# Kernel optimization log

Hardware: AMD Instinct MI355X
Metric: run time of the kernel (lower is better)

## Reference

```python
import jax, jax.numpy as jnp
import numpy as np

N = 100000
K = 16
C_IN = 64
C_MID = 64   # max(in_channels, out_channels // 2)
C_OUT = 128
EPS = 1e-5


def setup_inputs() -> dict:
    key = jax.random.key(0)
    ks = jax.random.split(key, 4)
    feat = jax.random.normal(ks[0], (N, C_IN), dtype=jnp.float32)
    reference_index = jax.random.randint(ks[1], (N, K), 0, N, dtype=jnp.int64)
    # Kaiming-ish init for the two Linear layers (torch Linear default scale)
    W1 = jax.random.normal(ks[2], (C_IN, C_MID), dtype=jnp.float32) / np.sqrt(C_IN)
    W2 = jax.random.normal(ks[3], (C_MID, C_OUT), dtype=jnp.float32) / np.sqrt(C_MID)
    return {
        "feat": feat,
        "reference_index": reference_index,
        "W1": W1,
        "b1": jnp.zeros((C_MID,), jnp.float32),
        "gamma1": jnp.ones((C_MID,), jnp.float32),
        "beta1": jnp.zeros((C_MID,), jnp.float32),
        "W2": W2,
        "b2": jnp.zeros((C_OUT,), jnp.float32),
        "gamma2": jnp.ones((C_OUT,), jnp.float32),
        "beta2": jnp.zeros((C_OUT,), jnp.float32),
    }


def _bn(x, gamma, beta):
    # BatchNorm1d in training mode: biased batch stats over the row dim.
    mean = jnp.mean(x, axis=0)
    var = jnp.var(x, axis=0)
    return (x - mean) * jax.lax.rsqrt(var + EPS) * gamma + beta


def reference(feat, reference_index, W1, b1, gamma1, beta1, W2, b2, gamma2, beta2):
    # grouping (with_xyz=False): gather neighbor features -> [N, K, C_IN]
    grouped = feat[reference_index]
    x = grouped.reshape(-1, C_IN)                 # [N*K, C_IN]
    h = jax.nn.relu(_bn(x @ W1 + b1, gamma1, beta1))   # [N*K, C_MID]
    h = jax.nn.relu(_bn(h @ W2 + b2, gamma2, beta2))   # [N*K, C_OUT]
    out = h.reshape(N, K, C_OUT).max(axis=1)      # max-pool over neighbors
    return out
```

## Files before the change

kernel.cpp:

```cpp
#include <hip/hip_runtime.h>
#include <hip/hip_bf16.h>

#define N_PTS 100000
#define KNN   16
#define NK    (N_PTS * KNN)
#define CIN   64
#define CMID  64
#define COUT  128

#define HSLC    64
#define SEG_CNT 25000
#define SEG_U32 12500

#define OFF_PC    0
#define OFF_HB    0
#define OFF_Z1B   25600000
#define OFF_CNT   38400000
#define OFF_STATS 38800000
#define OFF_W2BF  38801536
#define OFF_W1BF  38817920

typedef __attribute__((ext_vector_type(8))) short bf16x8;
typedef __attribute__((ext_vector_type(4))) float f32x4;
union U8 { uint4 u; bf16x8 v; unsigned short s[8]; };

__device__ __forceinline__ unsigned short f2bf(float f) {
    unsigned u = __float_as_uint(f);
    unsigned r = (u + 0x7fffu + ((u >> 16) & 1u)) >> 16;
    return (unsigned short)r;
}

__global__ __launch_bounds__(256) void hist_k(const int* __restrict__ idx,
                                              unsigned short* __restrict__ pc) {
    __shared__ unsigned int smem[SEG_U32];
    int seg  = blockIdx.x & 3;
    int slc  = blockIdx.x >> 2;
    int base = seg * SEG_CNT;

    for (int i = threadIdx.x; i < SEG_U32; i += 256) smem[i] = 0;
    __syncthreads();

    const int4* ip = (const int4*)idx;
    const int per = NK / 4 / HSLC;
    int s = slc * per, e = s + per;
    for (int i = s + threadIdx.x; i < e; i += 256) {
        int4 v = ip[i];
        int a;
        a = v.x - base; if ((unsigned)a < (unsigned)SEG_CNT)
            atomicAdd(&smem[a >> 1], 1u << ((a & 1) * 16));
        a = v.y - base; if ((unsigned)a < (unsigned)SEG_CNT)
            atomicAdd(&smem[a >> 1], 1u << ((a & 1) * 16));
        a = v.z - base; if ((unsigned)a < (unsigned)SEG_CNT)
            atomicAdd(&smem[a >> 1], 1u << ((a & 1) * 16));
        a = v.w - base; if ((unsigned)a < (unsigned)SEG_CNT)
            atomicAdd(&smem[a >> 1], 1u << ((a & 1) * 16));
    }
    __syncthreads();

    unsigned int* outp = (unsigned int*)(pc + (size_t)slc * N_PTS) + seg * SEG_U32;
    for (int i = threadIdx.x; i < SEG_U32; i += 256) outp[i] = smem[i];
}

__global__ __launch_bounds__(256) void sum_counts_k(const unsigned short* __restrict__ pc,
                                                    float* __restrict__ counts,
                                                    const float* __restrict__ W2,
                                                    unsigned short* __restrict__ w2bf,
                                                    const float* __restrict__ W1,
                                                    unsigned short* __restrict__ w1bf) {
    if (blockIdx.x == 196) {
        for (int e = threadIdx.x; e < 8192; e += 256) {
            int j = e & 7, lane = (e >> 3) & 63, kh = (e >> 9) & 1, nt = e >> 10;
            int k = kh * 32 + (lane >> 4) * 8 + j;
            int n = nt * 16 + (lane & 15);
            w2bf[e] = f2bf(W2[k * COUT + n]);
        }
        return;
    }
    if (blockIdx.x == 197) {
        for (int e = threadIdx.x; e < 4096; e += 256) {
            int j = e & 7, lane = (e >> 3) & 63, kh = (e >> 9) & 1, nt = e >> 10;
            int k = kh * 32 + (lane >> 4) * 8 + j;
            int n = nt * 16 + (lane & 15);
            w1bf[e] = f2bf(W1[k * CMID + n]);
        }
        return;
    }
    int i = blockIdx.x * 256 + threadIdx.x;
    if (i >= N_PTS / 2) return;
    const unsigned int* p = (const unsigned int*)pc;
    unsigned int u = 0;
    #pragma unroll
    for (int s = 0; s < HSLC; s++) u += p[s * (N_PTS / 2) + i];
    float2 r;
    r.x = (float)(u & 0xffffu);
    r.y = (float)(u >> 16);
    ((float2*)counts)[i] = r;
}

__global__ __launch_bounds__(256) void gemm1_k(const float* __restrict__ feat,
                                               const unsigned short* __restrict__ w1bf,
                                               const float* __restrict__ b1,
                                               const float* __restrict__ counts,
                                               unsigned short* __restrict__ z1b,
                                               float* __restrict__ S1,
                                               float* __restrict__ Q1) {
    int lane = threadIdx.x & 63, wid = threadIdx.x >> 6;
    int il = lane & 15, quad = lane >> 4;

    bf16x8 wf[4][2];
    const uint4* wp = (const uint4*)w1bf;
    #pragma unroll
    for (int nt = 0; nt < 4; nt++) {
        U8 t0; t0.u = wp[(nt * 2 + 0) * 64 + lane]; wf[nt][0] = t0.v;
        U8 t1; t1.u = wp[(nt * 2 + 1) * 64 + lane]; wf[nt][1] = t1.v;
    }
    float bias[4];
    #pragma unroll
    for (int nt = 0; nt < 4; nt++) bias[nt] = b1[nt * 16 + il];

    float s[4] = {0, 0, 0, 0}, q[4] = {0, 0, 0, 0};

    int wgid = blockIdx.x * 4 + wid;
    for (int tile = wgid; tile < N_PTS / 16; tile += gridDim.x * 4) {
        int m0 = tile * 16;
        const float* fr = feat + (size_t)(m0 + il) * 64;
        float4 fa = *(const float4*)(fr + quad * 8);
        float4 fb = *(const float4*)(fr + quad * 8 + 4);
        float4 fc = *(const float4*)(fr + 32 + quad * 8);
        float4 fd = *(const float4*)(fr + 32 + quad * 8 + 4);
        U8 ua, ub;
        ua.s[0] = f2bf(fa.x); ua.s[1] = f2bf(fa.y); ua.s[2] = f2bf(fa.z); ua.s[3] = f2bf(fa.w);
        ua.s[4] = f2bf(fb.x); ua.s[5] = f2bf(fb.y); ua.s[6] = f2bf(fb.z); ua.s[7] = f2bf(fb.w);
        ub.s[0] = f2bf(fc.x); ub.s[1] = f2bf(fc.y); ub.s[2] = f2bf(fc.z); ub.s[3] = f2bf(fc.w);
        ub.s[4] = f2bf(fd.x); ub.s[5] = f2bf(fd.y); ub.s[6] = f2bf(fd.z); ub.s[7] = f2bf(fd.w);

        float4 cnt4 = *(const float4*)(counts + m0 + quad * 4);
        #pragma unroll
        for (int nt = 0; nt < 4; nt++) {
            f32x4 acc = {bias[nt], bias[nt], bias[nt], bias[nt]};
            acc = __builtin_amdgcn_mfma_f32_16x16x32_bf16(ua.v, wf[nt][0], acc, 0, 0, 0);
            acc = __builtin_amdgcn_mfma_f32_16x16x32_bf16(ub.v, wf[nt][1], acc, 0, 0, 0);
            unsigned short* zp = z1b + (size_t)(m0 + quad * 4) * 64 + nt * 16 + il;
            zp[0]   = f2bf(acc[0]);
            zp[64]  = f2bf(acc[1]);
            zp[128] = f2bf(acc[2]);
            zp[192] = f2bf(acc[3]);
            s[nt] += cnt4.x * acc[0] + cnt4.y * acc[1] + cnt4.z * acc[2] + cnt4.w * acc[3];
            q[nt] += cnt4.x * acc[0] * acc[0] + cnt4.y * acc[1] * acc[1]
                   + cnt4.z * acc[2] * acc[2] + cnt4.w * acc[3] * acc[3];
        }
    }
    #pragma unroll
    for (int m = 16; m <= 32; m <<= 1) {
        #pragma unroll
        for (int nt = 0; nt < 4; nt++) {
            s[nt] += __shfl_xor(s[nt], m, 64);
            q[nt] += __shfl_xor(q[nt], m, 64);
        }
    }
    __shared__ float sred[2][4][4][16];
    if (quad == 0) {
        #pragma unroll
        for (int nt = 0; nt < 4; nt++) { sred[0][wid][nt][il] = s[nt]; sred[1][wid][nt][il] = q[nt]; }
    }
    __syncthreads();
    if (threadIdx.x < 128) {
        int which = threadIdx.x >> 6, c = threadIdx.x & 63;
        float t = sred[which][0][c >> 4][c & 15] + sred[which][1][c >> 4][c & 15]
                + sred[which][2][c >> 4][c & 15] + sred[which][3][c >> 4][c & 15];
        atomicAdd(which ? &Q1[c] : &S1[c], t);
    }
}

__device__ __forceinline__ bf16x8 bnrelu(uint4 r, float4 alo, float4 ahi,
                                         float4 blo, float4 bhi) {
    float z0 = __uint_as_float(r.x << 16), z1 = __uint_as_float(r.x & 0xffff0000u);
    float z2 = __uint_as_float(r.y << 16), z3 = __uint_as_float(r.y & 0xffff0000u);
    float z4 = __uint_as_float(r.z << 16), z5 = __uint_as_float(r.z & 0xffff0000u);
    float z6 = __uint_as_float(r.w << 16), z7 = __uint_as_float(r.w & 0xffff0000u);
    U8 o;
    o.s[0] = f2bf(fmaxf(fmaf(alo.x, z0, blo.x), 0.f));
    o.s[1] = f2bf(fmaxf(fmaf(alo.y, z1, blo.y), 0.f));
    o.s[2] = f2bf(fmaxf(fmaf(alo.z, z2, blo.z), 0.f));
    o.s[3] = f2bf(fmaxf(fmaf(alo.w, z3, blo.w), 0.f));
    o.s[4] = f2bf(fmaxf(fmaf(ahi.x, z4, bhi.x), 0.f));
    o.s[5] = f2bf(fmaxf(fmaf(ahi.y, z5, bhi.y), 0.f));
    o.s[6] = f2bf(fmaxf(fmaf(ahi.z, z6, bhi.z), 0.f));
    o.s[7] = f2bf(fmaxf(fmaf(ahi.w, z7, bhi.w), 0.f));
    return o.v;
}

__global__ __launch_bounds__(256) void stats2_k(const unsigned short* __restrict__ z1b,
                                                const unsigned short* __restrict__ w2bf,
                                                const float* __restrict__ S1,
                                                const float* __restrict__ Q1,
                                                const float* __restrict__ g1,
                                                const float* __restrict__ be1,
                                                const float* __restrict__ b2,
                                                const float* __restrict__ counts,
                                                unsigned short* __restrict__ hb,
                                                float* __restrict__ S2,
                                                float* __restrict__ Q2) {
    __shared__ float Al[64], Bl[64];
    if (threadIdx.x < 64) {
        const float inv = 1.0f / (float)NK;
        float m = S1[threadIdx.x] * inv;
        float v = Q1[threadIdx.x] * inv - m * m;
        float a = g1[threadIdx.x] * rsqrtf(v + 1e-5f);
        Al[threadIdx.x] = a;
        Bl[threadIdx.x] = be1[threadIdx.x] - m * a;
    }
    __syncthreads();

    int lane = threadIdx.x & 63, wid = threadIdx.x >> 6;
    int il = lane & 15, quad = lane >> 4;

    float4 a0lo = *(const float4*)(Al + quad * 8);
    float4 a0hi = *(const float4*)(Al + quad * 8 + 4);
    float4 b0lo = *(const float4*)(Bl + quad * 8);
    float4 b0hi = *(const float4*)(Bl + quad * 8 + 4);
    float4 a1lo = *(const float4*)(Al + 32 + quad * 8);
    float4 a1hi = *(const float4*)(Al + 32 + quad * 8 + 4);
    float4 b1lo = *(const float4*)(Bl + 32 + quad * 8);
    float4 b1hi = *(const float4*)(Bl + 32 + quad * 8 + 4);

    bf16x8 bfr[8][2];
    const uint4* wp = (const uint4*)w2bf;
    #pragma unroll
    for (int nt = 0; nt < 8; nt++) {
        U8 t0; t0.u = wp[(nt * 2 + 0) * 64 + lane]; bfr[nt][0] = t0.v;
        U8 t1; t1.u = wp[(nt * 2 + 1) * 64 + lane]; bfr[nt][1] = t1.v;
    }
    float bias[8];
    #pragma unroll
    for (int nt = 0; nt < 8; nt++) bias[nt] = b2[nt * 16 + il];

    float s[8], q[8];
    #pragma unroll
    for (int j = 0; j < 8; j++) { s[j] = 0.f; q[j] = 0.f; }

    int wgid = blockIdx.x * 4 + wid;
    for (int tile = wgid; tile < N_PTS / 16; tile += gridDim.x * 4) {
        int m0 = tile * 16;
        const uint4* ar = (const uint4*)(z1b + (size_t)(m0 + il) * 64);
        uint4 ra0 = ar[quad];
        uint4 ra1 = ar[4 + quad];
        bf16x8 af0 = bnrelu(ra0, a0lo, a0hi, b0lo, b0hi);
        bf16x8 af1 = bnrelu(ra1, a1lo, a1hi, b1lo, b1hi);
        U8 o0; o0.v = af0;
        U8 o1; o1.v = af1;
        uint4* hp = (uint4*)(hb + (size_t)(m0 + il) * 64);
        hp[quad]     = o0.u;
        hp[4 + quad] = o1.u;
        float4 cnt4 = *(const float4*)(counts + m0 + quad * 4);
        #pragma unroll
        for (int nt = 0; nt < 8; nt++) {
            f32x4 acc = {bias[nt], bias[nt], bias[nt], bias[nt]};
            acc = __builtin_amdgcn_mfma_f32_16x16x32_bf16(af0, bfr[nt][0], acc, 0, 0, 0);
            acc = __builtin_amdgcn_mfma_f32_16x16x32_bf16(af1, bfr[nt][1], acc, 0, 0, 0);
            s[nt] += cnt4.x * acc[0] + cnt4.y * acc[1] + cnt4.z * acc[2] + cnt4.w * acc[3];
            q[nt] += cnt4.x * acc[0] * acc[0] + cnt4.y * acc[1] * acc[1]
                   + cnt4.z * acc[2] * acc[2] + cnt4.w * acc[3] * acc[3];
        }
    }
    #pragma unroll
    for (int m = 16; m <= 32; m <<= 1) {
        #pragma unroll
        for (int nt = 0; nt < 8; nt++) {
            s[nt] += __shfl_xor(s[nt], m, 64);
            q[nt] += __shfl_xor(q[nt], m, 64);
        }
    }
    __shared__ float sred[2][4][8][16];
    if (quad == 0) {
        #pragma unroll
        for (int nt = 0; nt < 8; nt++) { sred[0][wid][nt][il] = s[nt]; sred[1][wid][nt][il] = q[nt]; }
    }
    __syncthreads();
    {
        int which = threadIdx.x >> 7, c = threadIdx.x & 127;
        float t = sred[which][0][c >> 4][c & 15] + sred[which][1][c >> 4][c & 15]
                + sred[which][2][c >> 4][c & 15] + sred[which][3][c >> 4][c & 15];
        atomicAdd(which ? &Q2[c] : &S2[c], t);
    }
}

__global__ __launch_bounds__(256) void fused_k(const unsigned short* __restrict__ hb,
                                               const unsigned short* __restrict__ w2bf,
                                               const int* __restrict__ idx,
                                               const float* __restrict__ b2,
                                               const float* __restrict__ S2,
                                               const float* __restrict__ Q2,
                                               const float* __restrict__ g2,
                                               const float* __restrict__ be2,
                                               float* __restrict__ out) {
    __shared__ float A2[128], B2f[128];
    __shared__ uint4 wlds[1024];

    for (int i = threadIdx.x; i < 1024; i += 256) wlds[i] = ((const uint4*)w2bf)[i];
    const float inv = 1.0f / (float)NK;
    if (threadIdx.x < 128) {
        int c = threadIdx.x;
        float m = S2[c] * inv;
        float v = Q2[c] * inv - m * m;
        float a = g2[c] * rsqrtf(v + 1e-5f);
        A2[c] = a;
        B2f[c] = fmaf(a, b2[c], be2[c] - m * a);
    }
    __syncthreads();

    int lane = threadIdx.x & 63, wid = threadIdx.x >> 6;
    int il = lane & 15, quad = lane >> 4;

    bf16x8 bfr[8][2];
    #pragma unroll
    for (int nt = 0; nt < 8; nt++) {
        U8 t0; t0.u = wlds[(nt * 2 + 0) * 64 + lane]; bfr[nt][0] = t0.v;
        U8 t1; t1.u = wlds[(nt * 2 + 1) * 64 + lane]; bfr[nt][1] = t1.v;
    }
    float a2c[8], b2c[8];
    #pragma unroll
    for (int nt = 0; nt < 8; nt++) {
        a2c[nt] = A2[nt * 16 + il];
        b2c[nt] = B2f[nt * 16 + il];
    }

    const int stride = gridDim.x * 4;
    int n  = blockIdx.x * 4 + wid;
    int n1 = n + stride;

    uint4 r0c = {0, 0, 0, 0}, r1c = {0, 0, 0, 0};
    if (n < N_PTS) {
        int j0 = idx[(size_t)n * KNN + il];
        const uint4* zr = (const uint4*)(hb + (size_t)j0 * 64);
        r0c = zr[quad];
        r1c = zr[4 + quad];
    }
    int j1 = (n1 < N_PTS) ? idx[(size_t)n1 * KNN + il] : 0;

    while (n < N_PTS) {
        uint4 r0n = {0, 0, 0, 0}, r1n = {0, 0, 0, 0};
        int n2 = n1 + stride;
        if (n1 < N_PTS) {
            const uint4* zr = (const uint4*)(hb + (size_t)j1 * 64);
            r0n = zr[quad];
            r1n = zr[4 + quad];
        }
        int j2 = (n2 < N_PTS) ? idx[(size_t)n2 * KNN + il] : 0;

        U8 ua, ub; ua.u = r0c; ub.u = r1c;
        float w0 = 0.f, w1 = 0.f;
        #pragma unroll
        for (int nt = 0; nt < 8; nt++) {
            f32x4 acc = {0.f, 0.f, 0.f, 0.f};
            acc = __builtin_amdgcn_mfma_f32_16x16x32_bf16(ua.v, bfr[nt][0], acc, 0, 0, 0);
            acc = __builtin_amdgcn_mfma_f32_16x16x32_bf16(ub.v, bfr[nt][1], acc, 0, 0, 0);
            float mx = fmaxf(fmaxf(acc[0], acc[1]), fmaxf(acc[2], acc[3]));
            float mn = fminf(fminf(acc[0], acc[1]), fminf(acc[2], acc[3]));
            mx = fmaxf(mx, __shfl_xor(mx, 16, 64));
            mn = fminf(mn, __shfl_xor(mn, 16, 64));
            mx = fmaxf(mx, __shfl_xor(mx, 32, 64));
            mn = fminf(mn, __shfl_xor(mn, 32, 64));
            float v = fmaxf(fmaxf(fmaf(a2c[nt], mx, b2c[nt]),
                                  fmaf(a2c[nt], mn, b2c[nt])), 0.f);
            if (nt == quad)     w0 = v;
            if (nt == quad + 4) w1 = v;
        }
        float* op = out + (size_t)n * COUT;
        __builtin_nontemporal_store(w0, op + quad * 16 + il);
        __builtin_nontemporal_store(w1, op + 64 + quad * 16 + il);

        n = n1; n1 = n2; j1 = j2;
        r0c = r0n; r1c = r1n;
    }
}

extern "C" void kernel_launch(void* const* d_in, const int* in_sizes, int n_in,
                              void* d_out, int out_size, void* d_ws, size_t ws_size,
                              hipStream_t stream) {
    const float* feat = (const float*)d_in[0];
    const int*   idx  = (const int*)d_in[1];
    const float* W1   = (const float*)d_in[2];
    const float* b1   = (const float*)d_in[3];
    const float* g1   = (const float*)d_in[4];
    const float* be1  = (const float*)d_in[5];
    const float* W2   = (const float*)d_in[6];
    const float* b2   = (const float*)d_in[7];
    const float* g2   = (const float*)d_in[8];
    const float* be2  = (const float*)d_in[9];
    float* out = (float*)d_out;

    char* ws = (char*)d_ws;
    unsigned short* pc  = (unsigned short*)(ws + OFF_PC);
    unsigned short* hb  = (unsigned short*)(ws + OFF_HB);
    unsigned short* z1b = (unsigned short*)(ws + OFF_Z1B);
    float* counts = (float*)(ws + OFF_CNT);
    float* S1 = (float*)(ws + OFF_STATS);
    float* Q1 = S1 + 64;
    float* S2 = S1 + 128;
    float* Q2 = S1 + 256;
    unsigned short* w2bf = (unsigned short*)(ws + OFF_W2BF);
    unsigned short* w1bf = (unsigned short*)(ws + OFF_W1BF);

    hipMemsetAsync(ws + OFF_STATS, 0, 1536, stream);

    hist_k<<<4 * HSLC, 256, 0, stream>>>(idx, pc);
    sum_counts_k<<<198, 256, 0, stream>>>(pc, counts, W2, w2bf, W1, w1bf);
    gemm1_k<<<512, 256, 0, stream>>>(feat, w1bf, b1, counts, z1b, S1, Q1);
    stats2_k<<<512, 256, 0, stream>>>(z1b, w2bf, S1, Q1, g1, be1, b2, counts, hb, S2, Q2);
    fused_k<<<1024, 256, 0, stream>>>(hb, w2bf, idx, b2, S2, Q2, g2, be2, out);
}
```

Baseline: 206.9 us.

## Fold BN2 scale sign into W2, drop min tracking, widen grids and histogram slices

Flips the sign of W2 columns whose BN2 scale is negative while loading them into LDS, then uses |scale|. The max-pool then needs only a running max, and the per-tile min reduction and its shuffles go away. It also doubles the histogram slice count, which halves contention per slice but doubles the partial-count buffer summed in sum_counts_k. Launch grids for gemm1, stats2 and fused are doubled. The LDS weight load now waits behind an extra barrier, and the larger slice count may overlap workspace regions and the 16-bit count limits.

```diff
diff --git a/kernel.cpp b/kernel.cpp
--- a/kernel.cpp
+++ b/kernel.cpp
@@ -8,7 +8,7 @@
 #define CMID  64
 #define COUT  128
 
-#define HSLC    64
+#define HSLC    128
 #define SEG_CNT 25000
 #define SEG_U32 12500
 
@@ -89,7 +89,7 @@
     if (i >= N_PTS / 2) return;
     const unsigned int* p = (const unsigned int*)pc;
     unsigned int u = 0;
-    #pragma unroll
+    #pragma unroll 32
     for (int s = 0; s < HSLC; s++) u += p[s * (N_PTS / 2) + i];
     float2 r;
     r.x = (float)(u & 0xffffu);
@@ -294,18 +294,28 @@
                                                const float* __restrict__ g2,
                                                const float* __restrict__ be2,
                                                float* __restrict__ out) {
-    __shared__ float A2[128], B2f[128];
+    __shared__ float A2s[128], B2f[128];
     __shared__ uint4 wlds[1024];
 
-    for (int i = threadIdx.x; i < 1024; i += 256) wlds[i] = ((const uint4*)w2bf)[i];
     const float inv = 1.0f / (float)NK;
     if (threadIdx.x < 128) {
         int c = threadIdx.x;
         float m = S2[c] * inv;
         float v = Q2[c] * inv - m * m;
         float a = g2[c] * rsqrtf(v + 1e-5f);
-        A2[c] = a;
+        A2s[c] = a;
         B2f[c] = fmaf(a, b2[c], be2[c] - m * a);
+    }
+    __syncthreads();
+
+    for (int i = threadIdx.x; i < 1024; i += 256) {
+        uint4 w = ((const uint4*)w2bf)[i];
+        int n_ = ((i >> 7) << 4) + (i & 15);
+        if (A2s[n_] < 0.f) {
+            w.x ^= 0x80008000u; w.y ^= 0x80008000u;
+            w.z ^= 0x80008000u; w.w ^= 0x80008000u;
+        }
+        wlds[i] = w;
     }
     __syncthreads();
 
@@ -321,7 +331,7 @@
     float a2c[8], b2c[8];
     #pragma unroll
     for (int nt = 0; nt < 8; nt++) {
-        a2c[nt] = A2[nt * 16 + il];
+        a2c[nt] = fabsf(A2s[nt * 16 + il]);
         b2c[nt] = B2f[nt * 16 + il];
     }
 
@@ -355,14 +365,10 @@
             f32x4 acc = {0.f, 0.f, 0.f, 0.f};
             acc = __builtin_amdgcn_mfma_f32_16x16x32_bf16(ua.v, bfr[nt][0], acc, 0, 0, 0);
             acc = __builtin_amdgcn_mfma_f32_16x16x32_bf16(ub.v, bfr[nt][1], acc, 0, 0, 0);
-            float mx = fmaxf(fmaxf(acc[0], acc[1]), fmaxf(acc[2], acc[3]));
-            float mn = fminf(fminf(acc[0], acc[1]), fminf(acc[2], acc[3]));
-            mx = fmaxf(mx, __shfl_xor(mx, 16, 64));
-            mn = fminf(mn, __shfl_xor(mn, 16, 64));
-            mx = fmaxf(mx, __shfl_xor(mx, 32, 64));
-            mn = fminf(mn, __shfl_xor(mn, 32, 64));
-            float v = fmaxf(fmaxf(fmaf(a2c[nt], mx, b2c[nt]),
-                                  fmaf(a2c[nt], mn, b2c[nt])), 0.f);
+            float t = fmaxf(fmaxf(acc[0], acc[1]), fmaxf(acc[2], acc[3]));
+            t = fmaxf(t, __shfl_xor(t, 16, 64));
+            t = fmaxf(t, __shfl_xor(t, 32, 64));
+            float v = fmaxf(fmaf(a2c[nt], t, b2c[nt]), 0.f);
             if (nt == quad)     w0 = v;
             if (nt == quad + 4) w1 = v;
         }
@@ -406,7 +412,7 @@
 
     hist_k<<<4 * HSLC, 256, 0, stream>>>(idx, pc);
     sum_counts_k<<<198, 256, 0, stream>>>(pc, counts, W2, w2bf, W1, w1bf);
-    gemm1_k<<<512, 256, 0, stream>>>(feat, w1bf, b1, counts, z1b, S1, Q1);
-    stats2_k<<<512, 256, 0, stream>>>(z1b, w2bf, S1, Q1, g1, be1, b2, counts, hb, S2, Q2);
-    fused_k<<<1024, 256, 0, stream>>>(hb, w2bf, idx, b2, S2, Q2, g2, be2, out);
-}
+    gemm1_k<<<1024, 256, 0, stream>>>(feat, w1bf, b1, counts, z1b, S1, Q1);
+    stats2_k<<<1024, 256, 0, stream>>>(z1b, w2bf, S1, Q1, g1, be1, b2, counts, hb, S2, Q2);
+    fused_k<<<2048, 256, 0, stream>>>(hb, w2bf, idx, b2, S2, Q2, g2, be2, out);
+}
```

Result: slower. 239.9 us (+15.9%).
